# Performance work log

Hardware: AMD Instinct MI355X
Metric: run time of the kernel (lower is better)

Reference implementation:

```python
import jax, jax.numpy as jnp
import numpy as np
import math

B, S, D, H = 4, 2048, 1024, 16
HD = D // H  # head dim = 64

def setup_inputs() -> dict:
    key = jax.random.key(0)
    ks = jax.random.split(key, 8)
    scale = 1.0 / math.sqrt(D)
    return {
        "hidden_states": jax.random.normal(ks[0], (B, S, D), jnp.float32),
        "attention_mask": jnp.zeros((B, 1, 1, S), jnp.float32),
        "Wq": jax.random.normal(ks[1], (D, D), jnp.float32) * scale,
        "bq": jnp.zeros((D,), jnp.float32),
        "Wk": jax.random.normal(ks[2], (D, D), jnp.float32) * scale,
        "bk": jnp.zeros((D,), jnp.float32),
        "Wv": jax.random.normal(ks[3], (D, D), jnp.float32) * scale,
        "bv": jnp.zeros((D,), jnp.float32),
    }

def _split_heads(x):
    # [B,S,D] -> [B,H,S,HD]
    return x.reshape(B, S, H, HD).transpose(0, 2, 1, 3)

def reference(hidden_states, attention_mask, Wq, bq, Wk, bk, Wv, bv):
    q = _split_heads(hidden_states @ Wq + bq)
    k = _split_heads(hidden_states @ Wk + bk)
    v = _split_heads(hidden_states @ Wv + bv)
    scores = jnp.einsum("bhqd,bhkd->bhqk", q, k) / math.sqrt(HD)
    scores = scores + attention_mask
    probs = jax.nn.softmax(scores, axis=-1)
    ctx = jnp.einsum("bhqk,bhkd->bhqd", probs, v)
    # [B,H,S,HD] -> [B,S,D]
    return ctx.transpose(0, 2, 1, 3).reshape(B, S, D)
```

## Files before the change

### kernel.cpp

```cpp
#include <hip/hip_runtime.h>
#include <hip/hip_bf16.h>
#include <stdint.h>

#define Bc 4
#define Sc 2048
#define Dc 1024
#define Hc 16
#define HDc 64
#define LOG2E 1.44269504088896f

typedef __attribute__((ext_vector_type(8))) __bf16 bf16x8;
typedef __attribute__((ext_vector_type(4))) __bf16 bf16x4;
typedef __attribute__((ext_vector_type(4))) float f32x4;
typedef __attribute__((ext_vector_type(16))) float f32x16;
typedef __attribute__((ext_vector_type(2))) int i32x2_t;

__device__ __forceinline__ f32x4 mfma16(bf16x8 a, bf16x8 b, f32x4 c) {
  return __builtin_amdgcn_mfma_f32_16x16x32_bf16(a, b, c, 0, 0, 0);
}
__device__ __forceinline__ f32x16 mfma32(bf16x8 a, bf16x8 b, f32x16 c) {
  return __builtin_amdgcn_mfma_f32_32x32x16_bf16(a, b, c, 0, 0, 0);
}
__device__ __forceinline__ uint32_t cvtpk_bf16(float lo, float hi) {
  uint32_t r;
  asm("v_cvt_pk_bf16_f32 %0, %1, %2" : "=v"(r) : "v"(lo), "v"(hi));
  return r;
}
__device__ __forceinline__ void gload_lds16(const void* g, void* l) {
  __builtin_amdgcn_global_load_lds(
      (const __attribute__((address_space(1))) void*)g,
      (__attribute__((address_space(3))) void*)l, 16, 0, 0);
}
__device__ __forceinline__ void gload_lds4(const void* g, void* l) {
  __builtin_amdgcn_global_load_lds(
      (const __attribute__((address_space(1))) void*)g,
      (__attribute__((address_space(3))) void*)l, 4, 0, 0);
}

__global__ __launch_bounds__(256) void prep_kernel(
    const float* __restrict__ hs, const float* __restrict__ mask,
    const float* __restrict__ Wq, const float* __restrict__ Wk,
    const float* __restrict__ Wv, __bf16* __restrict__ Ah,
    float* __restrict__ mkx, __bf16* __restrict__ Wt) {
  __shared__ float tile[64][65];
  const int bid = blockIdx.x;
  const int tid = threadIdx.x;
  if (bid < 32) {
    const int i = bid * 256 + tid;
    mkx[i] = mask[i] * LOG2E;
  } else if (bid < 4128) {
    const size_t i = ((size_t)(bid - 32) * 256 + tid) * 8;
    float4 f0 = *(const float4*)(hs + i);
    float4 f1 = *(const float4*)(hs + i + 4);
    bf16x8 o;
    o[0] = (__bf16)f0.x; o[1] = (__bf16)f0.y; o[2] = (__bf16)f0.z; o[3] = (__bf16)f0.w;
    o[4] = (__bf16)f1.x; o[5] = (__bf16)f1.y; o[6] = (__bf16)f1.z; o[7] = (__bf16)f1.w;
    *(bf16x8*)(Ah + i) = o;
  } else {
    const int u = bid - 4128;
    const int w = u >> 8;
    const int rem = u & 255;
    const int n0 = (rem & 15) * 64, k0 = (rem >> 4) * 64;
    const float* W = (w == 0) ? Wq : (w == 1 ? Wk : Wv);
    __bf16* out = Wt + (size_t)w * Dc * Dc;
    const int r = tid >> 2, cs = (tid & 3) * 16;
    const float* src = W + (size_t)(k0 + r) * Dc + n0 + cs;
    float4 f0 = *(const float4*)(src + 0);
    float4 f1 = *(const float4*)(src + 4);
    float4 f2 = *(const float4*)(src + 8);
    float4 f3 = *(const float4*)(src + 12);
#pragma unroll
    for (int j = 0; j < 4; ++j) {
      tile[r][cs + j] = ((const float*)&f0)[j];
      tile[r][cs + 4 + j] = ((const float*)&f1)[j];
      tile[r][cs + 8 + j] = ((const float*)&f2)[j];
      tile[r][cs + 12 + j] = ((const float*)&f3)[j];
    }
    __syncthreads();
    bf16x8 o0, o1;
#pragma unroll
    for (int j = 0; j < 8; ++j) {
      o0[j] = (__bf16)tile[cs + j][r];
      o1[j] = (__bf16)tile[cs + 8 + j][r];
    }
    __bf16* dst = out + (size_t)(n0 + r) * Dc + k0 + cs;
    *(bf16x8*)(dst) = o0;
    *(bf16x8*)(dst + 8) = o1;
  }
}

__global__ __launch_bounds__(512) void qkv_gemm_kernel(
    const __bf16* __restrict__ A, const __bf16* __restrict__ Wt,
    const float* __restrict__ bq, const float* __restrict__ bk,
    const float* __restrict__ bv,
    __bf16* __restrict__ Qo, __bf16* __restrict__ Kf, __bf16* __restrict__ Vf) {
  const int wg = (blockIdx.x & 7) * 96 + (blockIdx.x >> 3);
  const int nn = wg >> 6;
  const int mm = wg & 63;
  const int m0 = mm * 128;
  const int n0 = nn * 256;
  const int w = n0 >> 10;
  const int nbase = n0 & 1023;

  const float* bias = (w == 0) ? bq : (w == 1 ? bk : bv);

  __shared__ __attribute__((aligned(16))) __bf16 Asm[3][4096];
  __shared__ __attribute__((aligned(16))) __bf16 Bsm[3][8192];

  const int tid = threadIdx.x, lane = tid & 63, wid = tid >> 6;
  const int wr = wid >> 2, wc = wid & 3;
  const int lg = lane >> 4, li = lane & 15;

  f32x4 acc[4][4] = {};

  auto stage = [&](int buf, int kt) {
    const int k0 = kt * 32;
    {
      const int row = tid >> 2;
      const int sc = (tid & 3) ^ (row & 3);
      gload_lds16(A + (size_t)(m0 + row) * Dc + k0 + sc * 8,
                  &Asm[buf][wid * 512]);
    }
#pragma unroll
    for (int p = 0; p < 2; ++p) {
      const int row = p * 128 + (tid >> 2);
      const int sc = (tid & 3) ^ (row & 3);
      gload_lds16(Wt + (size_t)(n0 + row) * Dc + k0 + sc * 8,
                  &Bsm[buf][p * 4096 + wid * 512]);
    }
  };

  const int aoff = (wr * 64 + li) * 32 + ((lg ^ (li & 3)) * 8);
  const int boff = (wc * 64 + li) * 32 + ((lg ^ (li & 3)) * 8);

  stage(0, 0);
  stage(1, 1);
  for (int ks = 0; ks < 32; ++ks) {
    asm volatile("s_waitcnt vmcnt(3)" ::: "memory");
    __builtin_amdgcn_sched_barrier(0);
    __builtin_amdgcn_s_barrier();
    __builtin_amdgcn_sched_barrier(0);
    {
      const int tn = (ks + 2 < 32) ? ks + 2 : 31;
      stage((ks + 2) % 3, tn);
    }
    const __bf16* Ab = &Asm[ks % 3][0] + aoff;
    const __bf16* Bb = &Bsm[ks % 3][0] + boff;
    bf16x8 af[4], bfr[4];
#pragma unroll
    for (int i = 0; i < 4; ++i) af[i] = *(const bf16x8*)(Ab + i * 512);
#pragma unroll
    for (int j = 0; j < 4; ++j) bfr[j] = *(const bf16x8*)(Bb + j * 512);
    __builtin_amdgcn_s_setprio(1);
#pragma unroll
    for (int i = 0; i < 4; ++i)
#pragma unroll
      for (int j = 0; j < 4; ++j)
        acc[i][j] = mfma16(af[i], bfr[j], acc[i][j]);
    __builtin_amdgcn_s_setprio(0);
  }

  if (w == 0) {
    const float scl = 0.125f * LOG2E;
#pragma unroll
    for (int i = 0; i < 4; ++i) {
#pragma unroll
      for (int j = 0; j < 4; ++j) {
        const int n = nbase + wc * 64 + j * 16 + li;
        const float bb = bias[n];
        const int h = n >> 6, hd = n & 63;
#pragma unroll
        for (int r = 0; r < 4; ++r) {
          const int m = m0 + wr * 64 + i * 16 + lg * 4 + r;
          const int b = m >> 11, s = m & 2047;
          Qo[(((size_t)b * Hc + h) * Sc + s) * HDc + hd] =
              (__bf16)((acc[i][j][r] + bb) * scl);
        }
      }
    }
  } else if (w == 1) {
#pragma unroll
    for (int j = 0; j < 4; ++j) {
      const int n = nbase + wc * 64 + j * 16 + li;
      const float bb = bias[n];
      const int h = n >> 6, hd = n & 63;
      const int c = hd >> 4, shi = (hd >> 3) & 1, j8 = hd & 7;
#pragma unroll
      for (int i = 0; i < 4; ++i) {
#pragma unroll
        for (int r = 0; r < 4; ++r) {
          const int m = m0 + wr * 64 + i * 16 + lg * 4 + r;
          const int b = m >> 11, s = m & 2047;
          const int bh = b * Hc + h;
          const int t = s >> 6, kt = s & 63;
          const int slot = (kt >> 5) * 256 + c * 64 + shi * 32 + (kt & 31);
          Kf[((size_t)(bh * 32 + t)) * 4096 + slot * 8 + j8] =
              (__bf16)(acc[i][j][r] + bb);
        }
      }
    }
  } else {
#pragma unroll
    for (int i = 0; i < 4; ++i) {
      const int mbase = m0 + wr * 64 + i * 16 + lg * 4;
      const int b = mbase >> 11, sk = mbase & 2047;
      const int t = sk >> 6, kt = sk & 63;
      const int kc = kt >> 4, shi = (kt >> 3) & 1, j0 = kt & 7;
#pragma unroll
      for (int j = 0; j < 4; ++j) {
        const int n = nbase + wc * 64 + j * 16 + li;
        const float bb = bias[n];
        const int h = n >> 6, hd = n & 63;
        const int nb = hd >> 5, sqr = hd & 31;
        const int bh = b * Hc + h;
        const int slot = kc * 128 + nb * 64 + shi * 32 + sqr;
        bf16x4 o;
#pragma unroll
        for (int r = 0; r < 4; ++r) o[r] = (__bf16)(acc[i][j][r] + bb);
        *(bf16x4*)&Vf[((size_t)(bh * 32 + t)) * 4096 + slot * 8 + j0] = o;
      }
    }
  }
}

__global__ __launch_bounds__(512) void attn_kernel(
    const __bf16* __restrict__ Q, const __bf16* __restrict__ Kf,
    const __bf16* __restrict__ Vf, const float* __restrict__ mkx,
    float* __restrict__ out) {
  const int idx = blockIdx.x;
  const int bh = (idx & 7) | (((idx >> 3) & 7) << 3);
  const int qt = idx >> 6;
  const int b = bh >> 4, h = bh & 15;
  const __bf16* qb = Q + (size_t)bh * Sc * HDc;
  const __bf16* kfb = Kf + (size_t)bh * 32 * 4096;
  const __bf16* vfb = Vf + (size_t)bh * 32 * 4096;
  const float* mb = mkx + (size_t)b * Sc;

  const int tid = threadIdx.x, lane = tid & 63, wid = tid >> 6;
  const int hi = lane >> 5, qr = lane & 31;

  __shared__ __attribute__((aligned(16))) __bf16 Ksm[3][4096];
  __shared__ __attribute__((aligned(16))) __bf16 Vsm[3][4096];
  __shared__ __attribute__((aligned(16))) float Msm[3][64];

  const int q0 = qt * 256 + wid * 32;

  bf16x8 qf[4];
#pragma unroll
  for (int c = 0; c < 4; ++c)
    qf[c] = *(const bf16x8*)(qb + (size_t)(q0 + qr) * HDc + c * 16 + hi * 8);

  bf16x8 onesv;
#pragma unroll
  for (int j = 0; j < 8; ++j) onesv[j] = (__bf16)1.0f;

  f32x16 oacc[2] = {};
  f32x16 lacc = {};
  f32x16 sA[2], sB[2];

  auto stage = [&](int buf, int t) {
    const size_t tb = (size_t)t * 4096;
    gload_lds16(kfb + tb + (size_t)tid * 8, &Ksm[buf][wid * 512]);
    gload_lds16(vfb + tb + (size_t)tid * 8, &Vsm[buf][wid * 512]);
    gload_lds4(mb + t * 64 + lane, &Msm[buf][0]);
  };

  auto qk = [&](int buf, f32x16 (&s)[2]) {
    const __bf16* Kb = &Ksm[buf][0] + lane * 8;
    const float* Mb = &Msm[buf][0];
#pragma unroll
    for (int kb2 = 0; kb2 < 2; ++kb2) {
#pragma unroll
      for (int g = 0; g < 4; ++g) {
        const float4 m4 = *(const float4*)&Mb[kb2 * 32 + g * 8 + hi * 4];
#pragma unroll
        for (int e = 0; e < 4; ++e) s[kb2][g * 4 + e] = ((const float*)&m4)[e];
      }
    }
    __builtin_amdgcn_s_setprio(1);
#pragma unroll
    for (int kb2 = 0; kb2 < 2; ++kb2) {
#pragma unroll
      for (int c = 0; c < 4; ++c) {
        const bf16x8 kf = *(const bf16x8*)(Kb + (kb2 * 4 + c) * 512);
        s[kb2] = mfma32(kf, qf[c], s[kb2]);
      }
    }
    __builtin_amdgcn_s_setprio(0);
  };

  auto softpv = [&](int buf, f32x16 (&s)[2]) {
    const __bf16* Vb = &Vsm[buf][0] + lane * 8;
    bf16x8 pa[4];
#pragma unroll
    for (int kb2 = 0; kb2 < 2; ++kb2) {
      uint32_t wv[8];
#pragma unroll
      for (int j = 0; j < 8; ++j)
        wv[j] = cvtpk_bf16(__builtin_amdgcn_exp2f(s[kb2][2 * j]),
                           __builtin_amdgcn_exp2f(s[kb2][2 * j + 1]));
#pragma unroll
      for (int cc = 0; cc < 2; ++cc) {
        i32x2_t s02 = __builtin_amdgcn_permlane32_swap(
            (int)wv[cc * 4 + 0], (int)wv[cc * 4 + 2], false, false);
        i32x2_t s13 = __builtin_amdgcn_permlane32_swap(
            (int)wv[cc * 4 + 1], (int)wv[cc * 4 + 3], false, false);
        union { uint32_t u[4]; bf16x8 v; } af;
        af.u[0] = (uint32_t)s02[0];
        af.u[1] = (uint32_t)s13[0];
        af.u[2] = (uint32_t)s02[1];
        af.u[3] = (uint32_t)s13[1];
        pa[kb2 * 2 + cc] = af.v;
      }
    }
    __builtin_amdgcn_s_setprio(1);
#pragma unroll
    for (int kc = 0; kc < 4; ++kc) {
      lacc = mfma32(pa[kc], onesv, lacc);
#pragma unroll
      for (int nb = 0; nb < 2; ++nb) {
        const bf16x8 vf = *(const bf16x8*)(Vb + (kc * 2 + nb) * 512);
        oacc[nb] = mfma32(pa[kc], vf, oacc[nb]);
      }
    }
    __builtin_amdgcn_s_setprio(0);
  };

  const int NT = Sc / 64;

  stage(0, 0);
  stage(1, 1);
  __builtin_amdgcn_sched_barrier(0);
  asm volatile("s_waitcnt vmcnt(3)" ::: "memory");
  __builtin_amdgcn_s_barrier();
  __builtin_amdgcn_sched_barrier(0);
  qk(0, sA);

#define ITER(T, PB, QB, SB, CUR, NXT)                                   \
  {                                                                     \
    const int t_ = (T);                                                 \
    const int tn_ = (t_ + 2 < NT) ? t_ + 2 : NT - 1;                    \
    asm volatile("s_waitcnt vmcnt(0)" ::: "memory");                    \
    __builtin_amdgcn_sched_barrier(0);                                  \
    __builtin_amdgcn_s_barrier();                                       \
    __builtin_amdgcn_sched_barrier(0);                                  \
    stage(SB, tn_);                                                     \
    qk(QB, NXT);                                                        \
    softpv(PB, CUR);                                                    \
  }

  for (int t6 = 0; t6 < 30; t6 += 6) {
    ITER(t6 + 0, 0, 1, 2, sA, sB);
    ITER(t6 + 1, 1, 2, 0, sB, sA);
    ITER(t6 + 2, 2, 0, 1, sA, sB);
    ITER(t6 + 3, 0, 1, 2, sB, sA);
    ITER(t6 + 4, 1, 2, 0, sA, sB);
    ITER(t6 + 5, 2, 0, 1, sB, sA);
  }
  ITER(30, 0, 1, 2, sA, sB);
  ITER(31, 1, 2, 0, sB, sA);
#undef ITER

  float inv[16];
#pragma unroll
  for (int r = 0; r < 16; ++r) inv[r] = __builtin_amdgcn_rcpf(lacc[r]);
#pragma unroll
  for (int nb = 0; nb < 2; ++nb) {
#pragma unroll
    for (int r = 0; r < 16; ++r) {
      const int row = (r & 3) + 8 * (r >> 2) + 4 * hi;
      const int qg = q0 + row;
      out[((size_t)b * Sc + qg) * Dc + h * HDc + nb * 32 + qr] =
          oacc[nb][r] * inv[r];
    }
  }
}

extern "C" void kernel_launch(void* const* d_in, const int* in_sizes, int n_in,
                              void* d_out, int out_size, void* d_ws,
                              size_t ws_size, hipStream_t stream) {
  const float* hs = (const float*)d_in[0];
  const float* mask = (const float*)d_in[1];
  const float* Wq = (const float*)d_in[2];
  const float* bq = (const float*)d_in[3];
  const float* Wk = (const float*)d_in[4];
  const float* bk = (const float*)d_in[5];
  const float* Wv = (const float*)d_in[6];
  const float* bv = (const float*)d_in[7];
  float* out = (float*)d_out;

  char* ws = (char*)d_ws;
  const size_t qkv_bytes = (size_t)Bc * Hc * Sc * HDc * 2;
  __bf16* Wt = (__bf16*)ws;
  __bf16* Ah = (__bf16*)(ws + 6291456);
  __bf16* Q = (__bf16*)(ws + 6291456 + qkv_bytes);
  __bf16* Kf = (__bf16*)(ws + 6291456 + 2 * qkv_bytes);
  __bf16* Vf = (__bf16*)(ws + 6291456 + 3 * qkv_bytes);
  float* mkx = (float*)(ws + 6291456 + 4 * qkv_bytes);

  prep_kernel<<<4896, 256, 0, stream>>>(hs, mask, Wq, Wk, Wv, Ah, mkx, Wt);
  qkv_gemm_kernel<<<768, 512, 0, stream>>>(Ah, Wt, bq, bk, bv, Q, Kf, Vf);
  attn_kernel<<<512, 512, 0, stream>>>(Q, Kf, Vf, mkx, out);
}
```

Baseline: 168.9 us.

## Switch attention loop to double-buffered 128-key tiles without cross-iteration QK prefetch

Replaces the triple-buffered 64-key pipeline, where the QK for the next tile overlapped softmax/PV of the current one, with a double-buffered scheme loading 128 keys per stage and computing both halves' QK then both softmax/PV in the same iteration. This halves the number of barriers and waitcnt points per key, aiming to cut synchronisation overhead. The cost is that QK results are now consumed within the same iteration, with less software pipelining, and the load for the next tile lands right before it is needed. LDS use grows slightly.

```diff
diff --git a/kernel.cpp b/kernel.cpp
--- a/kernel.cpp
+++ b/kernel.cpp
@@ -239,9 +239,9 @@
   const int tid = threadIdx.x, lane = tid & 63, wid = tid >> 6;
   const int hi = lane >> 5, qr = lane & 31;
 
-  __shared__ __attribute__((aligned(16))) __bf16 Ksm[3][4096];
-  __shared__ __attribute__((aligned(16))) __bf16 Vsm[3][4096];
-  __shared__ __attribute__((aligned(16))) float Msm[3][64];
+  __shared__ __attribute__((aligned(16))) __bf16 Ksm[2][8192];
+  __shared__ __attribute__((aligned(16))) __bf16 Vsm[2][8192];
+  __shared__ __attribute__((aligned(16))) float Msm[2][128];
 
   const int q0 = qt * 256 + wid * 32;
 
@@ -256,18 +256,21 @@
 
   f32x16 oacc[2] = {};
   f32x16 lacc = {};
-  f32x16 sA[2], sB[2];
-
-  auto stage = [&](int buf, int t) {
-    const size_t tb = (size_t)t * 4096;
+  f32x16 s0[2], s1[2];
+
+  auto stage = [&](int buf, int T) {
+    const size_t tb = (size_t)(2 * T) * 4096;
     gload_lds16(kfb + tb + (size_t)tid * 8, &Ksm[buf][wid * 512]);
     gload_lds16(vfb + tb + (size_t)tid * 8, &Vsm[buf][wid * 512]);
-    gload_lds4(mb + t * 64 + lane, &Msm[buf][0]);
+    gload_lds16(kfb + tb + 4096 + (size_t)tid * 8, &Ksm[buf][4096 + wid * 512]);
+    gload_lds16(vfb + tb + 4096 + (size_t)tid * 8, &Vsm[buf][4096 + wid * 512]);
+    gload_lds4(mb + T * 128 + lane, &Msm[buf][0]);
+    gload_lds4(mb + T * 128 + 64 + lane, &Msm[buf][64]);
   };
 
-  auto qk = [&](int buf, f32x16 (&s)[2]) {
-    const __bf16* Kb = &Ksm[buf][0] + lane * 8;
-    const float* Mb = &Msm[buf][0];
+  auto qkh = [&](int buf, int half, f32x16 (&s)[2]) {
+    const __bf16* Kb = &Ksm[buf][half * 4096] + lane * 8;
+    const float* Mb = &Msm[buf][half * 64];
 #pragma unroll
     for (int kb2 = 0; kb2 < 2; ++kb2) {
 #pragma unroll
@@ -289,8 +292,8 @@
     __builtin_amdgcn_s_setprio(0);
   };
 
-  auto softpv = [&](int buf, f32x16 (&s)[2]) {
-    const __bf16* Vb = &Vsm[buf][0] + lane * 8;
+  auto softpvh = [&](int buf, int half, f32x16 (&s)[2]) {
+    const __bf16* Vb = &Vsm[buf][half * 4096] + lane * 8;
     bf16x8 pa[4];
 #pragma unroll
     for (int kb2 = 0; kb2 < 2; ++kb2) {
@@ -301,15 +304,15 @@
                            __builtin_amdgcn_exp2f(s[kb2][2 * j + 1]));
 #pragma unroll
       for (int cc = 0; cc < 2; ++cc) {
-        i32x2_t s02 = __builtin_amdgcn_permlane32_swap(
+        i32x2_t sw02 = __builtin_amdgcn_permlane32_swap(
             (int)wv[cc * 4 + 0], (int)wv[cc * 4 + 2], false, false);
-        i32x2_t s13 = __builtin_amdgcn_permlane32_swap(
+        i32x2_t sw13 = __builtin_amdgcn_permlane32_swap(
             (int)wv[cc * 4 + 1], (int)wv[cc * 4 + 3], false, false);
         union { uint32_t u[4]; bf16x8 v; } af;
-        af.u[0] = (uint32_t)s02[0];
-        af.u[1] = (uint32_t)s13[0];
-        af.u[2] = (uint32_t)s02[1];
-        af.u[3] = (uint32_t)s13[1];
+        af.u[0] = (uint32_t)sw02[0];
+        af.u[1] = (uint32_t)sw13[0];
+        af.u[2] = (uint32_t)sw02[1];
+        af.u[3] = (uint32_t)sw13[1];
         pa[kb2 * 2 + cc] = af.v;
       }
     }
@@ -326,39 +329,29 @@
     __builtin_amdgcn_s_setprio(0);
   };
 
-  const int NT = Sc / 64;
+  const int NT = Sc / 128;
 
   stage(0, 0);
-  stage(1, 1);
-  __builtin_amdgcn_sched_barrier(0);
-  asm volatile("s_waitcnt vmcnt(3)" ::: "memory");
-  __builtin_amdgcn_s_barrier();
-  __builtin_amdgcn_sched_barrier(0);
-  qk(0, sA);
-
-#define ITER(T, PB, QB, SB, CUR, NXT)                                   \
+
+#define ITER(T, PB, SB)                                                 \
   {                                                                     \
     const int t_ = (T);                                                 \
-    const int tn_ = (t_ + 2 < NT) ? t_ + 2 : NT - 1;                    \
+    const int tn_ = (t_ + 1 < NT) ? t_ + 1 : NT - 1;                    \
     asm volatile("s_waitcnt vmcnt(0)" ::: "memory");                    \
     __builtin_amdgcn_sched_barrier(0);                                  \
     __builtin_amdgcn_s_barrier();                                       \
     __builtin_amdgcn_sched_barrier(0);                                  \
     stage(SB, tn_);                                                     \
-    qk(QB, NXT);                                                        \
-    softpv(PB, CUR);                                                    \
-  }
-
-  for (int t6 = 0; t6 < 30; t6 += 6) {
-    ITER(t6 + 0, 0, 1, 2, sA, sB);
-    ITER(t6 + 1, 1, 2, 0, sB, sA);
-    ITER(t6 + 2, 2, 0, 1, sA, sB);
-    ITER(t6 + 3, 0, 1, 2, sB, sA);
-    ITER(t6 + 4, 1, 2, 0, sA, sB);
-    ITER(t6 + 5, 2, 0, 1, sB, sA);
-  }
-  ITER(30, 0, 1, 2, sA, sB);
-  ITER(31, 1, 2, 0, sB, sA);
+    qkh(PB, 0, s0);                                                     \
+    qkh(PB, 1, s1);                                                     \
+    softpvh(PB, 0, s0);                                                 \
+    softpvh(PB, 1, s1);                                                 \
+  }
+
+  for (int t2 = 0; t2 < NT; t2 += 2) {
+    ITER(t2 + 0, 0, 1);
+    ITER(t2 + 1, 1, 0);
+  }
 #undef ITER
 
   float inv[16];
```

Result: no change. 170.7 us (+1.1%).
